# Performance work log

Hardware: AMD Instinct MI355X
Metric: run time of the kernel (lower is better)

## Reference

```python
import jax, jax.numpy as jnp
import numpy as np
import math

D_MODEL = 1024
NUM_HEADS = 16
THETA = 10000.0


def _rope(x, pos):
    # x: [B, H, S, d_k]; pos: [S] int -- complex rotation on interleaved pairs
    d_k = x.shape[-1]
    inv_freq = 1.0 / (THETA ** (jnp.arange(0, d_k, 2, dtype=jnp.float32) / d_k))  # [d_k/2]
    angles = pos.astype(jnp.float32)[:, None] * inv_freq[None, :]  # [S, d_k/2]
    cos, sin = jnp.cos(angles), jnp.sin(angles)
    xe = x[..., 0::2]  # real parts
    xo = x[..., 1::2]  # imag parts
    out = jnp.stack([xe * cos - xo * sin, xe * sin + xo * cos], axis=-1)
    return out.reshape(x.shape)


def setup_inputs() -> dict:
    key = jax.random.key(0)
    k1, k2, k3 = jax.random.split(key, 3)
    B, S, D = 2, 2048, D_MODEL
    w_std = math.sqrt(2.0 / (D + 3 * D))
    o_std = math.sqrt(2.0 / (D + D))
    return {
        "x": jax.random.normal(k1, (B, S, D), dtype=jnp.float32),
        "token_positions": jnp.arange(S, dtype=jnp.int32),
        "w_qkv": jax.random.normal(k2, (3 * D, D), dtype=jnp.float32) * w_std,
        "w_out": jax.random.normal(k3, (D, D), dtype=jnp.float32) * o_std,
    }


def reference(x, token_positions, w_qkv, w_out):
    B, S, D = x.shape
    H = NUM_HEADS
    d_k = D // H

    qkv = jnp.einsum('bsd,ed->bse', x, w_qkv)  # [B, S, 3D]
    q, k, v = jnp.split(qkv, 3, axis=-1)

    def to_heads(t):
        return t.reshape(B, S, H, d_k).transpose(0, 2, 1, 3)  # [B, H, S, d_k]

    q, k, v = to_heads(q), to_heads(k), to_heads(v)
    q = _rope(q, token_positions)
    k = _rope(k, token_positions)

    scores = jnp.einsum('bhqd,bhkd->bhqk', q, k) / math.sqrt(d_k)
    causal = jnp.tril(jnp.ones((S, S), dtype=bool))
    scores = jnp.where(causal, scores, -jnp.inf)
    attn = jax.nn.softmax(scores, axis=-1)
    out = jnp.einsum('bhqk,bhkd->bhqd', attn, v)  # [B, H, S, d_k]
    out = out.transpose(0, 2, 1, 3).reshape(B, S, D)
    return jnp.einsum('bsd,ed->bse', out, w_out)
```

## Files before the change

### kernel.cpp

```cpp
#include <hip/hip_runtime.h>

typedef unsigned short u16;
typedef unsigned int u32;
typedef __attribute__((ext_vector_type(8))) __bf16 bf16x8;
typedef __attribute__((ext_vector_type(4))) float f32x4;
typedef __attribute__((ext_vector_type(4))) u32 u32x4;
typedef __attribute__((ext_vector_type(4))) u16 u16x4;

#define DEV __device__ __forceinline__

constexpr int S_LEN = 2048;
constexpr int DMODEL = 1024;
constexpr int NHEAD = 16;
constexpr int ROWS = 4096;
constexpr float QSCALE = 0.125f * 1.4426950408889634f;

DEV u16 f2bf(float f) {
  union { float f; u32 u; } v; v.f = f;
  u32 u = v.u;
  u32 r = (u + 0x7fffu + ((u >> 16) & 1u)) >> 16;
  return (u16)r;
}
DEV float vexp2(float x) {
#if __has_builtin(__builtin_amdgcn_exp2f)
  return __builtin_amdgcn_exp2f(x);
#else
  return exp2f(x);
#endif
}
DEV void gload_lds16(const u16* g, u16* l) {
  __builtin_amdgcn_global_load_lds((const __attribute__((address_space(1))) void*)g,
                                   (__attribute__((address_space(3))) void*)l, 16, 0, 0);
}
DEV int swz(int r, int c) { return r * 64 + (c ^ ((r & 7) << 3)); }

__global__ __launch_bounds__(256) void k_cvt_all(const float* __restrict__ x,
                                                 const float* __restrict__ wq,
                                                 const float* __restrict__ wo,
                                                 u16* __restrict__ xb,
                                                 u16* __restrict__ wqb,
                                                 u16* __restrict__ wob) {
  int i = blockIdx.x * 256 + threadIdx.x;
  const float* in; u16* out; int off;
  if (i < 524288)       { in = x;  out = xb;  off = i; }
  else if (i < 917504)  { in = wq; out = wqb; off = i - 524288; }
  else                  { in = wo; out = wob; off = i - 917504; }
  const float4* p4 = (const float4*)in;
  float4 a = p4[2 * off], b = p4[2 * off + 1];
  alignas(16) u16 r[8] = {f2bf(a.x), f2bf(a.y), f2bf(a.z), f2bf(a.w),
                          f2bf(b.x), f2bf(b.y), f2bf(b.z), f2bf(b.w)};
  *(u32x4*)(out + 8 * off) = *(const u32x4*)r;
}

__global__ __launch_bounds__(256) void k_rope_tab(const int* __restrict__ pos,
                                                  float2* __restrict__ tab) {
  int t = blockIdx.x * 256 + threadIdx.x;
  int s = t >> 5, fi = t & 31;
  float p = (float)pos[s];
  float invf = expf(-(float)fi * 0.28782313662425572f);
  float ang = p * invf;
  tab[t] = float2{cosf(ang), sinf(ang)};
}

template <int MODE>
__global__ __launch_bounds__(256, 2) void k_gemm(const u16* __restrict__ A,
                                                 const u16* __restrict__ Bw,
                                                 void* __restrict__ Out,
                                                 u16* __restrict__ vt,
                                                 const float2* __restrict__ tab,
                                                 int NB) {
  __shared__ alignas(16) u16 As[2][8192];
  __shared__ alignas(16) u16 Bs[2][8192];
  const int tid = threadIdx.x, lane = tid & 63;
  const int w = tid >> 6, wr = w >> 1, wc = w & 1;
  const int l15 = lane & 15, l16 = lane >> 4;
  const int cpx = gridDim.x >> 3;
  const int wg = (blockIdx.x & 7) * cpx + (blockIdx.x >> 3);
  const int mb = wg / NB, nb = wg - mb * NB;
  const int m0 = mb * 128, n0 = nb * 128;

  const int sr = tid >> 3;
  const int swcol = ((tid & 7) ^ (sr & 7)) * 8;
  const u16* aT = A + (size_t)(m0 + sr) * 1024 + swcol;
  const u16* bT = Bw + (size_t)(n0 + sr) * 1024 + swcol;
  const int dst0 = tid * 8;

#define STAGE(bufc, t) do { \
    _Pragma("unroll") \
    for (int i_ = 0; i_ < 4; i_++) { \
      gload_lds16(aT + (size_t)(i_ * 32) * 1024 + (t) * 64, &As[bufc][dst0 + i_ * 2048]); \
      gload_lds16(bT + (size_t)(i_ * 32) * 1024 + (t) * 64, &Bs[bufc][dst0 + i_ * 2048]); \
    } \
  } while (0)

  f32x4 acc[4][4] = {};
  const int x7 = l15 & 7;

#define COMPUTE(bufc) do { \
    bf16x8 af_[4][2], bf_[4][2]; \
    _Pragma("unroll") \
    for (int m_ = 0; m_ < 4; m_++) \
      _Pragma("unroll") \
      for (int k_ = 0; k_ < 2; k_++) \
        af_[m_][k_] = *(const bf16x8*)&As[bufc][(wr * 64 + m_ * 16 + l15) * 64 + \
                                               (((k_ * 4 + l16) ^ x7) * 8)]; \
    _Pragma("unroll") \
    for (int n_ = 0; n_ < 4; n_++) \
      _Pragma("unroll") \
      for (int k_ = 0; k_ < 2; k_++) \
        bf_[n_][k_] = *(const bf16x8*)&Bs[bufc][(wc * 64 + n_ * 16 + l15) * 64 + \
                                               (((k_ * 4 + l16) ^ x7) * 8)]; \
    __builtin_amdgcn_s_setprio(1); \
    _Pragma("unroll") \
    for (int m_ = 0; m_ < 4; m_++) \
      _Pragma("unroll") \
      for (int n_ = 0; n_ < 4; n_++) \
        _Pragma("unroll") \
        for (int k_ = 0; k_ < 2; k_++) \
          acc[m_][n_] = __builtin_amdgcn_mfma_f32_16x16x32_bf16( \
              af_[m_][k_], bf_[n_][k_], acc[m_][n_], 0, 0, 0); \
    __builtin_amdgcn_s_setprio(0); \
  } while (0)

  STAGE(0, 0);
  for (int t = 0; t < 16; ++t) {
    if (t + 1 < 16) {
      STAGE((t + 1) & 1, t + 1);
      asm volatile("s_waitcnt vmcnt(8)" ::: "memory");
    } else {
      asm volatile("s_waitcnt vmcnt(0)" ::: "memory");
    }
    asm volatile("s_barrier" ::: "memory");
    COMPUTE(t & 1);
    if (t + 1 < 16)
      asm volatile("s_barrier" ::: "memory");
  }
#undef STAGE
#undef COMPUTE

  const int rb = m0 + wr * 64 + l16 * 4;
  const int cb = n0 + wc * 64 + l15;
  if (MODE == 0) {
    float* o = (float*)Out;
#pragma unroll
    for (int m = 0; m < 4; m++)
#pragma unroll
      for (int n = 0; n < 4; n++)
#pragma unroll
        for (int r = 0; r < 4; r++)
          o[(size_t)(rb + m * 16 + r) * 1024 + cb + n * 16] = acc[m][n][r];
  } else if (n0 >= 2048) {
#pragma unroll
    for (int m = 0; m < 4; m++)
#pragma unroll
      for (int n = 0; n < 4; n++) {
        int row = rb + m * 16, col = cb + n * 16;
        int bb = row >> 11, s = row & 2047, hd = col - 2048;
        u16x4 pk = {f2bf(acc[m][n][0]), f2bf(acc[m][n][1]),
                    f2bf(acc[m][n][2]), f2bf(acc[m][n][3])};
        *(u16x4*)&vt[(size_t)(bb * 1024 + hd) * S_LEN + s] = pk;
      }
  } else {
    u16* qk = (u16*)Out;
    const bool isq = (n0 < 1024);
#pragma unroll
    for (int m = 0; m < 4; m++) {
      int row0 = rb + m * 16;
      int s0 = row0 & 2047;
#pragma unroll
      for (int n = 0; n < 4; n++) {
        int col = cb + n * 16;
        int fi = (col & 63) >> 1;
        bool odd = col & 1;
        f32x4 v = acc[m][n];
        f32x4 p;
#pragma unroll
        for (int r = 0; r < 4; r++) p[r] = __shfl_xor(v[r], 1);
#pragma unroll
        for (int r = 0; r < 4; r++) {
          float2 cs = tab[(s0 + r) * 32 + fi];
          float xe = odd ? p[r] : v[r];
          float xo = odd ? v[r] : p[r];
          float o = odd ? (xe * cs.y + xo * cs.x) : (xe * cs.x - xo * cs.y);
          if (isq) o *= QSCALE;
          qk[(size_t)(row0 + r) * 2048 + col] = f2bf(o);
        }
      }
    }
  }
}

__global__ __launch_bounds__(256) void k_attn(const u16* __restrict__ qk,
                                              const u16* __restrict__ vt,
                                              u16* __restrict__ aout) {
  __shared__ alignas(16) u16 Ks[64 * 64];
  __shared__ alignas(16) u16 Vs[64 * 64];
  __shared__ alignas(16) u16 Ps[4][16 * 64];
  const int tid = threadIdx.x, lane = tid & 63, w = tid >> 6;
  const int l15 = lane & 15, l16 = lane >> 4;
  const int qt = 31 - blockIdx.y;
  const int q0 = qt * 64;
  const int bh = blockIdx.x, b = bh >> 4, h = bh & 15;
  const u16* qbase = qk + (size_t)b * S_LEN * 2048 + h * 64;
  const u16* kbase = qbase + 1024;
  const u16* vbase = vt + (size_t)bh * 64 * S_LEN;
  const int wq0 = q0 + w * 16;

  bf16x8 qa[2];
#pragma unroll
  for (int kb = 0; kb < 2; kb++)
    qa[kb] = *(const bf16x8*)&qbase[(size_t)(wq0 + l15) * 2048 + kb * 32 + l16 * 8];

  bf16x8 vone;
#pragma unroll
  for (int j = 0; j < 8; j++) vone[j] = (__bf16)1.0f;

  f32x4 osum[4] = {};
  f32x4 osl = {};

  const int nt = qt + 1;
  const int srow = tid >> 2, scg = (tid & 3) * 16;
  u32x4 kr0, kr1, vr0, vr1;
  {
    const u16* kp = kbase + (size_t)srow * 2048 + scg;
    kr0 = *(const u32x4*)kp; kr1 = *(const u32x4*)(kp + 8);
    const u16* vp = vbase + (size_t)srow * S_LEN + scg;
    vr0 = *(const u32x4*)vp; vr1 = *(const u32x4*)(vp + 8);
  }

  for (int t = 0; t < nt; t++) {
    const int kv0 = t * 64;
    __syncthreads();
    *(u32x4*)&Ks[swz(srow, scg)]     = kr0;
    *(u32x4*)&Ks[swz(srow, scg + 8)] = kr1;
    *(u32x4*)&Vs[swz(srow, scg)]     = vr0;
    *(u32x4*)&Vs[swz(srow, scg + 8)] = vr1;
    __syncthreads();
    if (t + 1 < nt) {
      const u16* kp = kbase + (size_t)(kv0 + 64 + srow) * 2048 + scg;
      kr0 = *(const u32x4*)kp; kr1 = *(const u32x4*)(kp + 8);
      const u16* vp = vbase + (size_t)srow * S_LEN + kv0 + 64 + scg;
      vr0 = *(const u32x4*)vp; vr1 = *(const u32x4*)(vp + 8);
    }

    f32x4 sc[4];
#pragma unroll
    for (int n = 0; n < 4; n++) {
      bf16x8 kf0 = *(const bf16x8*)&Ks[swz(n * 16 + l15, l16 * 8)];
      bf16x8 kf1 = *(const bf16x8*)&Ks[swz(n * 16 + l15, 32 + l16 * 8)];
      f32x4 z = {0.f, 0.f, 0.f, 0.f};
      z = __builtin_amdgcn_mfma_f32_16x16x32_bf16(qa[0], kf0, z, 0, 0, 0);
      sc[n] = __builtin_amdgcn_mfma_f32_16x16x32_bf16(qa[1], kf1, z, 0, 0, 0);
    }

    const bool diag = (t == nt - 1);
#pragma unroll
    for (int n = 0; n < 4; n++)
#pragma unroll
      for (int r = 0; r < 4; r++) {
        float s = sc[n][r];
        if (diag && (kv0 + n * 16 + l15 > wq0 + l16 * 4 + r)) s = -1e30f;
        float p = vexp2(s - 16.0f);
        Ps[w][swz(l16 * 4 + r, n * 16 + l15)] = f2bf(p);
      }

#pragma unroll
    for (int ks = 0; ks < 2; ks++) {
      bf16x8 pa = *(const bf16x8*)&Ps[w][swz(l15, ks * 32 + l16 * 8)];
      osl = __builtin_amdgcn_mfma_f32_16x16x32_bf16(pa, vone, osl, 0, 0, 0);
#pragma unroll
      for (int n = 0; n < 4; n++) {
        bf16x8 vb = *(const bf16x8*)&Vs[swz(n * 16 + l15, ks * 32 + l16 * 8)];
        osum[n] = __builtin_amdgcn_mfma_f32_16x16x32_bf16(pa, vb, osum[n], 0, 0, 0);
      }
    }
  }

  f32x4 inv;
#pragma unroll
  for (int r = 0; r < 4; r++) inv[r] = 1.0f / osl[r];
  u16* ob = aout + (size_t)b * S_LEN * DMODEL + h * 64;
#pragma unroll
  for (int n = 0; n < 4; n++)
#pragma unroll
    for (int r = 0; r < 4; r++) {
      int s = wq0 + l16 * 4 + r;
      ob[(size_t)s * DMODEL + n * 16 + l15] = f2bf(osum[n][r] * inv[r]);
    }
}

extern "C" void kernel_launch(void* const* d_in, const int* in_sizes, int n_in,
                              void* d_out, int out_size, void* d_ws, size_t ws_size,
                              hipStream_t stream) {
  const float* x = (const float*)d_in[0];
  const int* pos = (const int*)d_in[1];
  const float* wqkv = (const float*)d_in[2];
  const float* wout = (const float*)d_in[3];
  float* out = (float*)d_out;
  char* ws = (char*)d_ws;

  u16* qkb   = (u16*)(ws);
  u16* vtb   = (u16*)(ws + 16777216);
  u16* aoutb = (u16*)(ws + 25165824);
  u16* xb    = (u16*)(ws + 33554432);
  u16* wqb   = (u16*)(ws + 41943040);
  u16* wob   = (u16*)(ws + 48234496);
  float2* tab = (float2*)(ws + 50331648);
  (void)ws_size;

  k_cvt_all<<<4096, 256, 0, stream>>>(x, wqkv, wout, xb, wqb, wob);
  k_rope_tab<<<65536 / 256, 256, 0, stream>>>(pos, tab);

  k_gemm<1><<<768, 256, 0, stream>>>(xb, wqb, qkb, vtb, tab, 24);

  dim3 ga(2 * NHEAD, S_LEN / 64);
  k_attn<<<ga, 256, 0, stream>>>(qkb, vtb, aoutb);

  k_gemm<0><<<256, 256, 0, stream>>>(aoutb, wob, out, nullptr, nullptr, 8);
}
```

Measured before the change: 109.0 us.

## Switch GEMM to register-staged loads with BK=32 and smaller output-projection tiles

The GEMM kernel no longer uses direct global-to-LDS loads with a 64-wide K tile. It now loads 32-wide K tiles into registers, writes them to swizzled LDS one step ahead, and uses a single barrier per iteration, with launch bounds raised to allow 4 blocks per CU. The output projection uses 64-row tiles, doubling its grid to 512 blocks so more CUs get work. The cost is twice as many K iterations and barriers, plus extra VGPR use for the staging registers.

```diff
diff --git a/kernel.cpp b/kernel.cpp
--- a/kernel.cpp
+++ b/kernel.cpp
@@ -27,10 +27,6 @@
 #else
   return exp2f(x);
 #endif
-}
-DEV void gload_lds16(const u16* g, u16* l) {
-  __builtin_amdgcn_global_load_lds((const __attribute__((address_space(1))) void*)g,
-                                   (__attribute__((address_space(3))) void*)l, 16, 0, 0);
 }
 DEV int swz(int r, int c) { return r * 64 + (c ^ ((r & 7) << 3)); }
 
@@ -62,88 +58,92 @@
   tab[t] = float2{cosf(ang), sinf(ang)};
 }
 
-template <int MODE>
-__global__ __launch_bounds__(256, 2) void k_gemm(const u16* __restrict__ A,
+template <int BM, int MODE>
+__global__ __launch_bounds__(256, 4) void k_gemm(const u16* __restrict__ A,
                                                  const u16* __restrict__ Bw,
                                                  void* __restrict__ Out,
                                                  u16* __restrict__ vt,
                                                  const float2* __restrict__ tab,
                                                  int NB) {
-  __shared__ alignas(16) u16 As[2][8192];
-  __shared__ alignas(16) u16 Bs[2][8192];
+  constexpr int MR = BM / 32;
+  constexpr int NA = BM / 64;
+  __shared__ alignas(16) u16 As[2][BM * 32];
+  __shared__ alignas(16) u16 Bs[2][128 * 32];
   const int tid = threadIdx.x, lane = tid & 63;
   const int w = tid >> 6, wr = w >> 1, wc = w & 1;
   const int l15 = lane & 15, l16 = lane >> 4;
   const int cpx = gridDim.x >> 3;
   const int wg = (blockIdx.x & 7) * cpx + (blockIdx.x >> 3);
   const int mb = wg / NB, nb = wg - mb * NB;
-  const int m0 = mb * 128, n0 = nb * 128;
-
-  const int sr = tid >> 3;
-  const int swcol = ((tid & 7) ^ (sr & 7)) * 8;
-  const u16* aT = A + (size_t)(m0 + sr) * 1024 + swcol;
-  const u16* bT = Bw + (size_t)(n0 + sr) * 1024 + swcol;
-  const int dst0 = tid * 8;
-
-#define STAGE(bufc, t) do { \
+  const int m0 = mb * BM, n0 = nb * 128;
+
+  const int grow = tid >> 2, gc = tid & 3;
+  const u16* aP = A + (size_t)(m0 + grow) * 1024 + gc * 8;
+  const u16* bP = Bw + (size_t)(n0 + grow) * 1024 + gc * 8;
+  const int wrI = grow * 32 + ((gc ^ (grow & 3)) << 3);
+
+  u32x4 ra0, ra1, rb0, rb1;
+#define LOADT(t) do { \
+    ra0 = *(const u32x4*)(aP + (t) * 32); \
+    if (NA == 2) ra1 = *(const u32x4*)(aP + 65536 + (t) * 32); \
+    rb0 = *(const u32x4*)(bP + (t) * 32); \
+    rb1 = *(const u32x4*)(bP + 65536 + (t) * 32); \
+  } while (0)
+#define WRITET(bufc) do { \
+    *(u32x4*)&As[bufc][wrI] = ra0; \
+    if (NA == 2) *(u32x4*)&As[bufc][wrI + 2048] = ra1; \
+    *(u32x4*)&Bs[bufc][wrI] = rb0; \
+    *(u32x4*)&Bs[bufc][wrI + 2048] = rb1; \
+  } while (0)
+
+  f32x4 acc[MR][4] = {};
+  const int x3 = l15 & 3;
+
+#define COMPUTE(bufc) do { \
+    bf16x8 af[MR]; \
     _Pragma("unroll") \
-    for (int i_ = 0; i_ < 4; i_++) { \
-      gload_lds16(aT + (size_t)(i_ * 32) * 1024 + (t) * 64, &As[bufc][dst0 + i_ * 2048]); \
-      gload_lds16(bT + (size_t)(i_ * 32) * 1024 + (t) * 64, &Bs[bufc][dst0 + i_ * 2048]); \
-    } \
-  } while (0)
-
-  f32x4 acc[4][4] = {};
-  const int x7 = l15 & 7;
-
-#define COMPUTE(bufc) do { \
-    bf16x8 af_[4][2], bf_[4][2]; \
-    _Pragma("unroll") \
-    for (int m_ = 0; m_ < 4; m_++) \
-      _Pragma("unroll") \
-      for (int k_ = 0; k_ < 2; k_++) \
-        af_[m_][k_] = *(const bf16x8*)&As[bufc][(wr * 64 + m_ * 16 + l15) * 64 + \
-                                               (((k_ * 4 + l16) ^ x7) * 8)]; \
-    _Pragma("unroll") \
-    for (int n_ = 0; n_ < 4; n_++) \
-      _Pragma("unroll") \
-      for (int k_ = 0; k_ < 2; k_++) \
-        bf_[n_][k_] = *(const bf16x8*)&Bs[bufc][(wc * 64 + n_ * 16 + l15) * 64 + \
-                                               (((k_ * 4 + l16) ^ x7) * 8)]; \
+    for (int m_ = 0; m_ < MR; m_++) \
+      af[m_] = *(const bf16x8*)&As[bufc][(wr * (BM / 2) + m_ * 16 + l15) * 32 + \
+                                         (((l16 ^ x3)) << 3)]; \
     __builtin_amdgcn_s_setprio(1); \
     _Pragma("unroll") \
-    for (int m_ = 0; m_ < 4; m_++) \
+    for (int n_ = 0; n_ < 4; n_++) { \
+      bf16x8 bb = *(const bf16x8*)&Bs[bufc][(wc * 64 + n_ * 16 + l15) * 32 + \
+                                            (((l16 ^ x3)) << 3)]; \
       _Pragma("unroll") \
-      for (int n_ = 0; n_ < 4; n_++) \
-        _Pragma("unroll") \
-        for (int k_ = 0; k_ < 2; k_++) \
-          acc[m_][n_] = __builtin_amdgcn_mfma_f32_16x16x32_bf16( \
-              af_[m_][k_], bf_[n_][k_], acc[m_][n_], 0, 0, 0); \
+      for (int m_ = 0; m_ < MR; m_++) \
+        acc[m_][n_] = __builtin_amdgcn_mfma_f32_16x16x32_bf16(af[m_], bb, acc[m_][n_], 0, 0, 0); \
+    } \
     __builtin_amdgcn_s_setprio(0); \
   } while (0)
 
-  STAGE(0, 0);
-  for (int t = 0; t < 16; ++t) {
-    if (t + 1 < 16) {
-      STAGE((t + 1) & 1, t + 1);
-      asm volatile("s_waitcnt vmcnt(8)" ::: "memory");
-    } else {
-      asm volatile("s_waitcnt vmcnt(0)" ::: "memory");
-    }
-    asm volatile("s_barrier" ::: "memory");
+#define BAR() do { \
+    asm volatile("s_waitcnt lgkmcnt(0)" ::: "memory"); \
+    __builtin_amdgcn_s_barrier(); \
+  } while (0)
+
+  LOADT(0);
+  WRITET(0);
+  LOADT(1);
+  BAR();
+
+  for (int t = 0; t < 32; ++t) {
     COMPUTE(t & 1);
-    if (t + 1 < 16)
-      asm volatile("s_barrier" ::: "memory");
+    if (t + 1 < 32) WRITET((t + 1) & 1);
+    if (t + 2 < 32) LOADT(t + 2);
+    BAR();
   }
-#undef STAGE
+#undef LOADT
+#undef WRITET
 #undef COMPUTE
-
-  const int rb = m0 + wr * 64 + l16 * 4;
+#undef BAR
+
+  const int rb = m0 + wr * (BM / 2) + l16 * 4;
   const int cb = n0 + wc * 64 + l15;
   if (MODE == 0) {
     float* o = (float*)Out;
 #pragma unroll
-    for (int m = 0; m < 4; m++)
+    for (int m = 0; m < MR; m++)
 #pragma unroll
       for (int n = 0; n < 4; n++)
 #pragma unroll
@@ -151,7 +151,7 @@
           o[(size_t)(rb + m * 16 + r) * 1024 + cb + n * 16] = acc[m][n][r];
   } else if (n0 >= 2048) {
 #pragma unroll
-    for (int m = 0; m < 4; m++)
+    for (int m = 0; m < MR; m++)
 #pragma unroll
       for (int n = 0; n < 4; n++) {
         int row = rb + m * 16, col = cb + n * 16;
@@ -164,7 +164,7 @@
     u16* qk = (u16*)Out;
     const bool isq = (n0 < 1024);
 #pragma unroll
-    for (int m = 0; m < 4; m++) {
+    for (int m = 0; m < MR; m++) {
       int row0 = rb + m * 16;
       int s0 = row0 & 2047;
 #pragma unroll
@@ -311,10 +311,10 @@
   k_cvt_all<<<4096, 256, 0, stream>>>(x, wqkv, wout, xb, wqb, wob);
   k_rope_tab<<<65536 / 256, 256, 0, stream>>>(pos, tab);
 
-  k_gemm<1><<<768, 256, 0, stream>>>(xb, wqb, qkb, vtb, tab, 24);
+  k_gemm<128, 1><<<768, 256, 0, stream>>>(xb, wqb, qkb, vtb, tab, 24);
 
   dim3 ga(2 * NHEAD, S_LEN / 64);
   k_attn<<<ga, 256, 0, stream>>>(qkb, vtb, aoutb);
 
-  k_gemm<0><<<256, 256, 0, stream>>>(aoutb, wob, out, nullptr, nullptr, 8);
-}
+  k_gemm<64, 0><<<512, 256, 0, stream>>>(aoutb, wob, out, nullptr, nullptr, 8);
+}
```

Result: faster. 102.2 us (-6.2%).

## Switch GEMMs to 256x256 tiles with 8 waves and interleaved staged loads

Applied to the files above, without the earlier changes.

Replaces the 128x128, 4-wave GEMM with a 256x256-tile, 512-thread, 8-wave kernel. Global-to-LDS loads are split into half-tile stages and interleaved with four MFMA quarter-steps per K iteration, with barriers between them. This raises operand reuse per LDS byte and overlaps loading with compute. The cost is far fewer workgroups (192 and 64 on a 256-CU part), which leaves many CUs idle, plus doubled LDS use (128KB) and extra barriers.

```diff
diff --git a/kernel.cpp b/kernel.cpp
--- a/kernel.cpp
+++ b/kernel.cpp
@@ -63,87 +63,120 @@
 }
 
 template <int MODE>
-__global__ __launch_bounds__(256, 2) void k_gemm(const u16* __restrict__ A,
-                                                 const u16* __restrict__ Bw,
-                                                 void* __restrict__ Out,
-                                                 u16* __restrict__ vt,
-                                                 const float2* __restrict__ tab,
-                                                 int NB) {
-  __shared__ alignas(16) u16 As[2][8192];
-  __shared__ alignas(16) u16 Bs[2][8192];
+__global__ __launch_bounds__(512, 2) void k_gemm8(const u16* __restrict__ A,
+                                                  const u16* __restrict__ Bw,
+                                                  void* __restrict__ Out,
+                                                  u16* __restrict__ vt,
+                                                  const float2* __restrict__ tab,
+                                                  int NB) {
+  __shared__ alignas(16) u16 As[2][16384];
+  __shared__ alignas(16) u16 Bs[2][16384];
   const int tid = threadIdx.x, lane = tid & 63;
-  const int w = tid >> 6, wr = w >> 1, wc = w & 1;
+  const int w = tid >> 6, wr = w >> 2, wc = w & 3;
   const int l15 = lane & 15, l16 = lane >> 4;
   const int cpx = gridDim.x >> 3;
   const int wg = (blockIdx.x & 7) * cpx + (blockIdx.x >> 3);
   const int mb = wg / NB, nb = wg - mb * NB;
-  const int m0 = mb * 128, n0 = nb * 128;
-
-  const int sr = tid >> 3;
-  const int swcol = ((tid & 7) ^ (sr & 7)) * 8;
-  const u16* aT = A + (size_t)(m0 + sr) * 1024 + swcol;
-  const u16* bT = Bw + (size_t)(n0 + sr) * 1024 + swcol;
-  const int dst0 = tid * 8;
-
-#define STAGE(bufc, t) do { \
+  const int m0 = mb * 256, n0 = nb * 256;
+
+  const int str = tid >> 3;
+  const int gd = tid & 7;
+  const int gs = gd ^ (str & 7);
+  const u16* aS = A + (size_t)(m0 + str) * 1024 + gs * 8;
+  const u16* bS = Bw + (size_t)(n0 + str) * 1024 + gs * 8;
+  const int dI = str * 64 + gd * 8;
+
+#define STGA(T, h) do { \
+    gload_lds16(aS + (size_t)((h) * 128) * 1024 + (T) * 64, &As[(T) & 1][(h) * 8192 + dI]); \
+    gload_lds16(aS + (size_t)((h) * 128 + 64) * 1024 + (T) * 64, \
+                &As[(T) & 1][(h) * 8192 + 4096 + dI]); \
+  } while (0)
+#define STGB(T, h) do { \
+    gload_lds16(bS + (size_t)((h) * 128) * 1024 + (T) * 64, &Bs[(T) & 1][(h) * 8192 + dI]); \
+    gload_lds16(bS + (size_t)((h) * 128 + 64) * 1024 + (T) * 64, \
+                &Bs[(T) & 1][(h) * 8192 + 4096 + dI]); \
+  } while (0)
+
+  f32x4 acc[8][4] = {};
+  const int xr = l15 & 7;
+  const int rofs0 = ((l16 ^ xr)) * 8;
+  const int rofs1 = (((4 + l16) ^ xr)) * 8;
+  bf16x8 Af[2][4][2], Bf[2][2];
+
+#define RDA(mq) do { \
     _Pragma("unroll") \
-    for (int i_ = 0; i_ < 4; i_++) { \
-      gload_lds16(aT + (size_t)(i_ * 32) * 1024 + (t) * 64, &As[bufc][dst0 + i_ * 2048]); \
-      gload_lds16(bT + (size_t)(i_ * 32) * 1024 + (t) * 64, &Bs[bufc][dst0 + i_ * 2048]); \
+    for (int m_ = 0; m_ < 4; m_++) { \
+      const u16* p_ = &As[b][(wr * 128 + (mq) * 64 + m_ * 16 + l15) * 64]; \
+      Af[mq][m_][0] = *(const bf16x8*)(p_ + rofs0); \
+      Af[mq][m_][1] = *(const bf16x8*)(p_ + rofs1); \
     } \
   } while (0)
-
-  f32x4 acc[4][4] = {};
-  const int x7 = l15 & 7;
-
-#define COMPUTE(bufc) do { \
-    bf16x8 af_[4][2], bf_[4][2]; \
+#define RDB(nq) do { \
     _Pragma("unroll") \
-    for (int m_ = 0; m_ < 4; m_++) \
-      _Pragma("unroll") \
-      for (int k_ = 0; k_ < 2; k_++) \
-        af_[m_][k_] = *(const bf16x8*)&As[bufc][(wr * 64 + m_ * 16 + l15) * 64 + \
-                                               (((k_ * 4 + l16) ^ x7) * 8)]; \
-    _Pragma("unroll") \
-    for (int n_ = 0; n_ < 4; n_++) \
-      _Pragma("unroll") \
-      for (int k_ = 0; k_ < 2; k_++) \
-        bf_[n_][k_] = *(const bf16x8*)&Bs[bufc][(wc * 64 + n_ * 16 + l15) * 64 + \
-                                               (((k_ * 4 + l16) ^ x7) * 8)]; \
+    for (int n_ = 0; n_ < 2; n_++) { \
+      const u16* p_ = &Bs[b][(wc * 64 + (nq) * 32 + n_ * 16 + l15) * 64]; \
+      Bf[n_][0] = *(const bf16x8*)(p_ + rofs0); \
+      Bf[n_][1] = *(const bf16x8*)(p_ + rofs1); \
+    } \
+  } while (0)
+#define MF(mq, nq) do { \
     __builtin_amdgcn_s_setprio(1); \
     _Pragma("unroll") \
     for (int m_ = 0; m_ < 4; m_++) \
       _Pragma("unroll") \
-      for (int n_ = 0; n_ < 4; n_++) \
+      for (int n_ = 0; n_ < 2; n_++) \
         _Pragma("unroll") \
         for (int k_ = 0; k_ < 2; k_++) \
-          acc[m_][n_] = __builtin_amdgcn_mfma_f32_16x16x32_bf16( \
-              af_[m_][k_], bf_[n_][k_], acc[m_][n_], 0, 0, 0); \
+          acc[(mq) * 4 + m_][(nq) * 2 + n_] = __builtin_amdgcn_mfma_f32_16x16x32_bf16( \
+              Af[mq][m_][k_], Bf[n_][k_], acc[(mq) * 4 + m_][(nq) * 2 + n_], 0, 0, 0); \
     __builtin_amdgcn_s_setprio(0); \
   } while (0)
-
-  STAGE(0, 0);
-  for (int t = 0; t < 16; ++t) {
-    if (t + 1 < 16) {
-      STAGE((t + 1) & 1, t + 1);
-      asm volatile("s_waitcnt vmcnt(8)" ::: "memory");
-    } else {
-      asm volatile("s_waitcnt vmcnt(0)" ::: "memory");
-    }
-    asm volatile("s_barrier" ::: "memory");
-    COMPUTE(t & 1);
-    if (t + 1 < 16)
-      asm volatile("s_barrier" ::: "memory");
+#define BARRIER() __builtin_amdgcn_s_barrier()
+#define LGKM0() asm volatile("s_waitcnt lgkmcnt(0)" ::: "memory")
+
+  STGA(0, 0); STGA(0, 1); STGB(0, 0); STGB(0, 1);
+  STGA(1, 0); STGA(1, 1);
+  asm volatile("s_waitcnt vmcnt(4)" ::: "memory");
+  BARRIER();
+
+  for (int T = 0; T < 16; ++T) {
+    const int b = T & 1;
+    if (T + 1 < 16) STGB(T + 1, 0);
+    RDA(0); RDB(0);
+    BARRIER(); LGKM0();
+    MF(0, 0);
+    BARRIER();
+    if (T + 1 < 16) STGB(T + 1, 1);
+    RDA(1);
+    BARRIER(); LGKM0();
+    MF(1, 0);
+    BARRIER();
+    if (T + 2 < 16) STGA(T + 2, 0);
+    RDB(1);
+    BARRIER(); LGKM0();
+    MF(0, 1);
+    BARRIER();
+    if (T + 2 < 16) STGA(T + 2, 1);
+    if (T < 13) asm volatile("s_waitcnt vmcnt(4)" ::: "memory");
+    else        asm volatile("s_waitcnt vmcnt(0)" ::: "memory");
+    BARRIER();
+    MF(1, 1);
+    BARRIER();
   }
-#undef STAGE
-#undef COMPUTE
-
-  const int rb = m0 + wr * 64 + l16 * 4;
+#undef STGA
+#undef STGB
+#undef RDA
+#undef RDB
+#undef MF
+#undef BARRIER
+#undef LGKM0
+
+  const int rb = m0 + wr * 128 + l16 * 4;
   const int cb = n0 + wc * 64 + l15;
   if (MODE == 0) {
     float* o = (float*)Out;
 #pragma unroll
-    for (int m = 0; m < 4; m++)
+    for (int m = 0; m < 8; m++)
 #pragma unroll
       for (int n = 0; n < 4; n++)
 #pragma unroll
@@ -151,7 +184,7 @@
           o[(size_t)(rb + m * 16 + r) * 1024 + cb + n * 16] = acc[m][n][r];
   } else if (n0 >= 2048) {
 #pragma unroll
-    for (int m = 0; m < 4; m++)
+    for (int m = 0; m < 8; m++)
 #pragma unroll
       for (int n = 0; n < 4; n++) {
         int row = rb + m * 16, col = cb + n * 16;
@@ -164,7 +197,7 @@
     u16* qk = (u16*)Out;
     const bool isq = (n0 < 1024);
 #pragma unroll
-    for (int m = 0; m < 4; m++) {
+    for (int m = 0; m < 8; m++) {
       int row0 = rb + m * 16;
       int s0 = row0 & 2047;
 #pragma unroll
@@ -311,10 +344,10 @@
   k_cvt_all<<<4096, 256, 0, stream>>>(x, wqkv, wout, xb, wqb, wob);
   k_rope_tab<<<65536 / 256, 256, 0, stream>>>(pos, tab);
 
-  k_gemm<1><<<768, 256, 0, stream>>>(xb, wqb, qkb, vtb, tab, 24);
+  k_gemm8<1><<<192, 512, 0, stream>>>(xb, wqb, qkb, vtb, tab, 12);
 
   dim3 ga(2 * NHEAD, S_LEN / 64);
   k_attn<<<ga, 256, 0, stream>>>(qkb, vtb, aoutb);
 
-  k_gemm<0><<<256, 256, 0, stream>>>(aoutb, wob, out, nullptr, nullptr, 8);
-}
+  k_gemm8<0><<<64, 512, 0, stream>>>(aoutb, wob, out, nullptr, nullptr, 4);
+}
```

New measurement: 135.0 us. 23.8% more time.
